# Kernel tuning notes

Hardware: AMD Instinct MI355X
Metric: run time of the kernel (lower is better)

The kernel has to match this reference:

```python
import jax, jax.numpy as jnp
import numpy as np

B, N, C = 2, 4096, 1024
HEADS = 16
BUCKET = 64
N_HASHES = 4
DH = C // HEADS
TOKEN_SELF_ATTN_VALUE = -5e4  # self-attention strongly discouraged (shared QK)


def setup_inputs() -> dict:
    key = jax.random.key(0)
    ks = jax.random.split(key, 8)
    s = 0.02
    n_buckets = N // BUCKET
    return {
        "queries": jax.random.normal(ks[0], (B, N, C), jnp.float32),
        "keys": jax.random.normal(ks[1], (B, N, C), jnp.float32),
        "values": jax.random.normal(ks[2], (B, N, C), jnp.float32),
        "attn_mask": jnp.zeros((1,), jnp.float32),
        "Wqk": jax.random.normal(ks[3], (C, C), jnp.float32) * s,
        "Wv": jax.random.normal(ks[4], (C, C), jnp.float32) * s,
        "Wout": jax.random.normal(ks[5], (C, C), jnp.float32) * s,
        "bout": jnp.zeros((C,), jnp.float32),
        # LSH random rotations, shared across batch and heads (reformer_pytorch default)
        "rotations": jax.random.normal(ks[6], (DH, N_HASHES, n_buckets // 2), jnp.float32),
        "tau": 1,
        "delta": 1,
    }


def _look_one_back(x):
    # concat each chunk with the previous chunk (wrap-around), along the kv axis
    extra = jnp.concatenate([x[:, -1:], x[:, :-1]], axis=1)
    return jnp.concatenate([x, extra], axis=2)


def _lsh_attention(qk, v, rotations, bucket_size, n_hashes):
    # qk, v: (bh, t, d); rotations: (d, n_hashes, n_buckets//2)
    bh, t, d = qk.shape
    n_buckets = t // bucket_size

    # --- hash vectors into buckets ---
    rotated = jnp.einsum('btf,fhi->bhti', qk, rotations)
    rotated = jnp.concatenate([rotated, -rotated], axis=-1)      # (bh, H, t, n_buckets)
    buckets = jnp.argmax(rotated, axis=-1)                       # (bh, H, t)
    offsets = (jnp.arange(n_hashes) * n_buckets)[None, :, None]
    buckets = (buckets + offsets).reshape(bh, n_hashes * t)

    # --- stable sort tokens by (bucket, position) ---
    ticker = jnp.arange(n_hashes * t)
    buckets_and_t = t * buckets + (ticker % t)[None, :]
    sticker = jnp.argsort(buckets_and_t, axis=-1)                # stable
    undo_sort = jnp.argsort(sticker, axis=-1)
    st = sticker % t                                             # original token idx per slot

    sqk = jnp.take_along_axis(qk, st[:, :, None], axis=1)
    sv = jnp.take_along_axis(v, st[:, :, None], axis=1)

    # --- chunk into n_hashes*n_buckets chunks of bucket_size ---
    n_chunks = n_hashes * n_buckets
    bq_t = st.reshape(bh, n_chunks, bucket_size)
    bqk = sqk.reshape(bh, n_chunks, bucket_size, d)
    bv = sv.reshape(bh, n_chunks, bucket_size, d)

    bq = bqk
    norm = jnp.linalg.norm(bqk, axis=-1, keepdims=True)
    bk = bqk / jnp.maximum(norm, 1e-12)                          # F.normalize, shared QK

    bk = _look_one_back(bk)
    bv = _look_one_back(bv)
    bkv_t = _look_one_back(bq_t)

    dots = jnp.einsum('bcie,bcje->bcij', bq, bk) * (d ** -0.5)   # (bh, nc, bs, 2*bs)
    self_mask = bq_t[..., :, None] == bkv_t[..., None, :]
    dots = jnp.where(self_mask, TOKEN_SELF_ATTN_VALUE, dots)

    dots_lse = jax.nn.logsumexp(dots, axis=-1, keepdims=True)
    probs = jnp.exp(dots - dots_lse)
    bo = jnp.einsum('bcij,bcje->bcie', probs, bv)

    # --- unsort and combine hash rounds by softmax over per-round logsumexps ---
    so = bo.reshape(bh, n_hashes * t, d)
    slogits = dots_lse.reshape(bh, n_hashes * t)
    o = jnp.take_along_axis(so, undo_sort[:, :, None], axis=1)
    logits = jnp.take_along_axis(slogits, undo_sort, axis=1)
    o = o.reshape(bh, n_hashes, t, d)
    logits = logits.reshape(bh, n_hashes, t, 1)
    w = jnp.exp(logits - jax.nn.logsumexp(logits, axis=1, keepdims=True))
    return jnp.sum(o * w, axis=1)                                # (bh, t, d)


def _forward(queries, Wqk, Wv, Wout, bout, rotations):
    b, n, c = queries.shape
    pad = (-n) % (BUCKET * 2)
    x = jnp.pad(queries, ((0, 0), (0, pad), (0, 0))) if pad else queries
    t = x.shape[1]
    qk = x @ Wqk.T
    v = x @ Wv.T
    qkh = qk.reshape(b, t, HEADS, DH).transpose(0, 2, 1, 3).reshape(b * HEADS, t, DH)
    vh = v.reshape(b, t, HEADS, DH).transpose(0, 2, 1, 3).reshape(b * HEADS, t, DH)
    oh = _lsh_attention(qkh, vh, rotations, BUCKET, N_HASHES)
    o = oh.reshape(b, HEADS, t, DH).transpose(0, 2, 1, 3).reshape(b, t, c)
    out = o @ Wout.T + bout
    return out[:, :n, :]


def reference(queries, keys, values, attn_mask, Wqk, Wv, Wout, bout, rotations, tau, delta):
    # keys/values/attn_mask/tau/delta are accepted but unused, as in the original layer
    return _forward(queries, Wqk, Wv, Wout, bout, rotations)
```

## Files before the change

kernel.cpp:

```cpp
#include <hip/hip_runtime.h>
#include <hip/hip_bf16.h>
#include <math.h>


__global__ __launch_bounds__(256) void sgemm128(const float* __restrict__ A,
                                                const float* __restrict__ W,
                                                float* __restrict__ out,
                                                int headLayout,
                                                const float* __restrict__ bias) {
    __shared__ float As[8][128];
    __shared__ float Bs[8][128];
    int tid = threadIdx.x;
    int tx = tid & 15, ty = tid >> 4;
    int m0 = blockIdx.x * 128, n0 = blockIdx.y * 128;
    int lr = tid >> 1;
    int lk = (tid & 1) * 4;
    float acc[8][8];
#pragma unroll
    for (int i = 0; i < 8; ++i)
#pragma unroll
        for (int j = 0; j < 8; ++j) acc[i][j] = 0.f;

    for (int k0 = 0; k0 < 1024; k0 += 8) {
        float4 av = *(const float4*)&A[(size_t)(m0 + lr) * 1024 + k0 + lk];
        float4 bv = *(const float4*)&W[(size_t)(n0 + lr) * 1024 + k0 + lk];
        __syncthreads();
        As[lk + 0][lr] = av.x; As[lk + 1][lr] = av.y;
        As[lk + 2][lr] = av.z; As[lk + 3][lr] = av.w;
        Bs[lk + 0][lr] = bv.x; Bs[lk + 1][lr] = bv.y;
        Bs[lk + 2][lr] = bv.z; Bs[lk + 3][lr] = bv.w;
        __syncthreads();
#pragma unroll
        for (int kk = 0; kk < 8; ++kk) {
            float a[8], b[8];
            *(float4*)&a[0] = *(const float4*)&As[kk][tx * 8];
            *(float4*)&a[4] = *(const float4*)&As[kk][tx * 8 + 4];
            *(float4*)&b[0] = *(const float4*)&Bs[kk][ty * 8];
            *(float4*)&b[4] = *(const float4*)&Bs[kk][ty * 8 + 4];
#pragma unroll
            for (int i = 0; i < 8; ++i)
#pragma unroll
                for (int j = 0; j < 8; ++j)
                    acc[i][j] = fmaf(a[i], b[j], acc[i][j]);
        }
    }
#pragma unroll
    for (int i = 0; i < 8; ++i) {
        int m = m0 + tx * 8 + i;
        int bb = m >> 12, t = m & 4095;
#pragma unroll
        for (int j = 0; j < 8; ++j) {
            int n = n0 + ty * 8 + j;
            float val = acc[i][j];
            if (bias) val += bias[n];
            if (headLayout) {
                out[(((size_t)(bb * 16 + (n >> 6))) * 4096 + t) * 64 + (n & 63)] = val;
            } else {
                out[(size_t)m * 1024 + n] = val;
            }
        }
    }
}

__global__ __launch_bounds__(256) void bucket32(const float* __restrict__ qk,
                                                const float* __restrict__ rot,
                                                int* __restrict__ keys) {
    int gid = blockIdx.x * 256 + threadIdx.x;
    int token = gid & 4095;
    int r = (gid >> 12) & 3;
    int bh = gid >> 14;
    const float* q = &qk[((size_t)bh * 4096 + token) * 64];
    float racc[32];
#pragma unroll
    for (int i = 0; i < 32; ++i) racc[i] = 0.f;
    for (int f = 0; f < 64; ++f) {
        float qv = q[f];
        const float* rp = &rot[f * 128 + r * 32];
#pragma unroll
        for (int i = 0; i < 32; ++i) racc[i] = fmaf(qv, rp[i], racc[i]);
    }
    float best = -INFINITY;
    int bi = 0;
#pragma unroll
    for (int i = 0; i < 32; ++i) { if (racc[i] > best) { best = racc[i]; bi = i; } }
#pragma unroll
    for (int i = 0; i < 32; ++i) { float x = -racc[i]; if (x > best) { best = x; bi = 32 + i; } }
    int bin = r * 64 + bi;
    keys[(size_t)bh * 16384 + r * 4096 + token] = bin * 4096 + token;
}

#define PST 257

__global__ __launch_bounds__(256) void countsort_kernel(const int* __restrict__ keys,
                                                        int* __restrict__ st_sorted) {
    __shared__ unsigned short pre[64 * PST];
    __shared__ unsigned char sbin[4096];
    __shared__ unsigned short sperm[4096];
    __shared__ int qsum[64 * 4];
    __shared__ int qoff[64 * 4];
    __shared__ int binOffset[64];

    int tid = threadIdx.x;
    int bh = blockIdx.x >> 2;
    int r = blockIdx.x & 3;
    const int* kb = &keys[(((size_t)bh * 4 + r) << 12)];

    for (int u = tid; u < 64 * PST; u += 256) pre[u] = 0;
    __syncthreads();

    int base = tid << 4;
#pragma unroll
    for (int u = 0; u < 4; ++u) {
        int4 kv = *(const int4*)&kb[base + u * 4];
        int b0 = (kv.x >> 12) & 63;
        int b1 = (kv.y >> 12) & 63;
        int b2 = (kv.z >> 12) & 63;
        int b3 = (kv.w >> 12) & 63;
        sbin[base + u * 4 + 0] = (unsigned char)b0;
        sbin[base + u * 4 + 1] = (unsigned char)b1;
        sbin[base + u * 4 + 2] = (unsigned char)b2;
        sbin[base + u * 4 + 3] = (unsigned char)b3;
        pre[b0 * PST + tid]++;
        pre[b1 * PST + tid]++;
        pre[b2 * PST + tid]++;
        pre[b3 * PST + tid]++;
    }
    __syncthreads();

    int b = tid & 63, q = tid >> 6;
    {
        int run = 0;
        for (int i = 0; i < 64; ++i) run += pre[b * PST + q * 64 + i];
        qsum[b * 4 + q] = run;
    }
    __syncthreads();

    if (tid < 64) {
        int s0 = qsum[tid * 4 + 0], s1 = qsum[tid * 4 + 1];
        int s2 = qsum[tid * 4 + 2], s3 = qsum[tid * 4 + 3];
        qoff[tid * 4 + 0] = 0;
        qoff[tid * 4 + 1] = s0;
        qoff[tid * 4 + 2] = s0 + s1;
        qoff[tid * 4 + 3] = s0 + s1 + s2;
        binOffset[tid] = s0 + s1 + s2 + s3;
    }
    __syncthreads();
    if (tid == 0) {
        int running = 0;
        for (int i = 0; i < 64; ++i) {
            int t = binOffset[i];
            binOffset[i] = running;
            running += t;
        }
    }
    __syncthreads();

    {
        int run2 = qoff[b * 4 + q];
        for (int i = 0; i < 64; ++i) {
            int idx = b * PST + q * 64 + i;
            int t = pre[idx];
            pre[idx] = (unsigned short)run2;
            run2 += t;
        }
    }
    __syncthreads();

#pragma unroll
    for (int k = 0; k < 16; ++k) {
        int bin = sbin[base + k];
        int off = pre[bin * PST + tid]++;
        sperm[binOffset[bin] + off] = (unsigned short)(base + k);
    }
    __syncthreads();

    int* ob = &st_sorted[(((size_t)bh * 4 + r) << 12)];
#pragma unroll
    for (int u = 0; u < 16; ++u) ob[u * 256 + tid] = (int)sperm[u * 256 + tid];
}

__global__ __launch_bounds__(256) void attn_kernel(const float* __restrict__ qk,
                                                   const float* __restrict__ v,
                                                   const int* __restrict__ st_sorted,
                                                   float* __restrict__ o4,
                                                   float* __restrict__ lse4) {
    __shared__ float bufA[128 * 68];
    __shared__ float vsl[128 * 68];
    __shared__ float red[64 * 17];
    __shared__ int posl[128];
    __shared__ float invl[128];

    int tid = threadIdx.x;
    int bh = blockIdx.x >> 8;
    int c = blockIdx.x & 255;
    int r = c >> 6;
    int pc = (c + 255) & 255;
    const int* stb = &st_sorted[(size_t)bh * 16384];
    if (tid < 64) posl[tid] = stb[c * 64 + tid];
    else if (tid < 128) posl[tid] = stb[pc * 64 + (tid - 64)];
    __syncthreads();

    float* kqt = bufA;
    for (int u = 0; u < 8; ++u) {
        int flat = u * 256 + tid;
        int row = flat >> 4;
        int f4 = (flat & 15) * 4;
        size_t gbase = ((size_t)bh * 4096 + posl[row]) * 64 + f4;
        float4 qv = *(const float4*)&qk[gbase];
        kqt[(f4 + 0) * 132 + row] = qv.x;
        kqt[(f4 + 1) * 132 + row] = qv.y;
        kqt[(f4 + 2) * 132 + row] = qv.z;
        kqt[(f4 + 3) * 132 + row] = qv.w;
        *(float4*)&vsl[row * 68 + f4] = *(const float4*)&v[gbase];
    }
    __syncthreads();

    if (tid < 128) {
        float ss = 0.f;
        for (int f = 0; f < 64; ++f) { float x = kqt[f * 132 + tid]; ss += x * x; }
        invl[tid] = 1.0f / fmaxf(sqrtf(ss), 1e-12f);
    }
    __syncthreads();

    int tx = tid & 15, ty = tid >> 4;
    float acc[4][8];
#pragma unroll
    for (int i = 0; i < 4; ++i)
#pragma unroll
        for (int j = 0; j < 8; ++j) acc[i][j] = 0.f;
    for (int f = 0; f < 64; ++f) {
        float a[4], b[8];
        *(float4*)a = *(const float4*)&kqt[f * 132 + tx * 4];
        *(float4*)&b[0] = *(const float4*)&kqt[f * 132 + ty * 8];
        *(float4*)&b[4] = *(const float4*)&kqt[f * 132 + ty * 8 + 4];
#pragma unroll
        for (int i = 0; i < 4; ++i)
#pragma unroll
            for (int j = 0; j < 8; ++j) acc[i][j] = fmaf(a[i], b[j], acc[i][j]);
    }

    int qp[4];
#pragma unroll
    for (int ii = 0; ii < 4; ++ii) qp[ii] = posl[tx * 4 + ii];
#pragma unroll
    for (int jj = 0; jj < 8; ++jj) {
        int j = ty * 8 + jj;
        float sc = invl[j] * 0.125f;
        int kp = posl[j];
#pragma unroll
        for (int ii = 0; ii < 4; ++ii) {
            float x = acc[ii][jj] * sc;
            acc[ii][jj] = (qp[ii] == kp) ? -5e4f : x;
        }
    }

#pragma unroll
    for (int ii = 0; ii < 4; ++ii) {
        float pm = acc[ii][0];
#pragma unroll
        for (int jj = 1; jj < 8; ++jj) pm = fmaxf(pm, acc[ii][jj]);
        red[(tx * 4 + ii) * 17 + ty] = pm;
    }
    __syncthreads();
    float m[4];
#pragma unroll
    for (int ii = 0; ii < 4; ++ii) {
        float mm = red[(tx * 4 + ii) * 17 + 0];
        for (int t = 1; t < 16; ++t) mm = fmaxf(mm, red[(tx * 4 + ii) * 17 + t]);
        m[ii] = mm;
    }
    __syncthreads();

    float* pT = bufA;
    float ps[4] = {0.f, 0.f, 0.f, 0.f};
#pragma unroll
    for (int jj = 0; jj < 8; ++jj) {
        int j = ty * 8 + jj;
#pragma unroll
        for (int ii = 0; ii < 4; ++ii) {
            float e = __expf(acc[ii][jj] - m[ii]);
            pT[j * 68 + tx * 4 + ii] = e;
            ps[ii] += e;
        }
    }
#pragma unroll
    for (int ii = 0; ii < 4; ++ii) red[(tx * 4 + ii) * 17 + ty] = ps[ii];
    __syncthreads();
    float l[4];
#pragma unroll
    for (int ii = 0; ii < 4; ++ii) {
        float s = 0.f;
        for (int t = 0; t < 16; ++t) s += red[(tx * 4 + ii) * 17 + t];
        l[ii] = s;
    }

    if (ty == 0) {
#pragma unroll
        for (int ii = 0; ii < 4; ++ii) {
            int i = tx * 4 + ii;
            lse4[((size_t)bh * 4 + r) * 4096 + posl[i]] = m[ii] + __logf(l[ii]);
        }
    }

    float acc2[4][4];
#pragma unroll
    for (int i = 0; i < 4; ++i)
#pragma unroll
        for (int j = 0; j < 4; ++j) acc2[i][j] = 0.f;
    for (int j = 0; j < 128; ++j) {
        float a[4], b[4];
        *(float4*)a = *(const float4*)&pT[j * 68 + tx * 4];
        *(float4*)b = *(const float4*)&vsl[j * 68 + ty * 4];
#pragma unroll
        for (int ii = 0; ii < 4; ++ii)
#pragma unroll
            for (int cc = 0; cc < 4; ++cc) acc2[ii][cc] = fmaf(a[ii], b[cc], acc2[ii][cc]);
    }
#pragma unroll
    for (int ii = 0; ii < 4; ++ii) {
        int i = tx * 4 + ii;
        float rl = 1.0f / l[ii];
        size_t ob = (((size_t)bh * 4 + r) * 4096 + posl[i]) * 64 + ty * 4;
        float4 ov;
        ov.x = acc2[ii][0] * rl;
        ov.y = acc2[ii][1] * rl;
        ov.z = acc2[ii][2] * rl;
        ov.w = acc2[ii][3] * rl;
        *(float4*)&o4[ob] = ov;
    }
}

__global__ __launch_bounds__(256) void combine_kernel(const float* __restrict__ o4,
                                                      const float* __restrict__ lse4,
                                                      float* __restrict__ o_bt) {
    int tid = threadIdx.x;
    int gt = blockIdx.x * 4 + (tid >> 6);
    int d = tid & 63;
    int bh = gt >> 12, p = gt & 4095;
    size_t base = ((size_t)bh * 4) * 4096 + p;
    float l0 = lse4[base];
    float l1 = lse4[base + 4096];
    float l2 = lse4[base + 8192];
    float l3 = lse4[base + 12288];
    float mm = fmaxf(fmaxf(l0, l1), fmaxf(l2, l3));
    float w0 = __expf(l0 - mm), w1 = __expf(l1 - mm);
    float w2 = __expf(l2 - mm), w3 = __expf(l3 - mm);
    float W = w0 + w1 + w2 + w3;
    size_t ob = (((size_t)bh * 4) * 4096 + p) * 64 + d;
    const size_t rs = (size_t)4096 * 64;
    float o = w0 * o4[ob]
            + w1 * o4[ob + rs]
            + w2 * o4[ob + 2 * rs]
            + w3 * o4[ob + 3 * rs];
    int b = bh >> 4, h = bh & 15;
    o_bt[((size_t)b * 4096 + p) * 1024 + h * 64 + d] = o / W;
}

extern "C" void kernel_launch(void* const* d_in, const int* in_sizes, int n_in,
                              void* d_out, int out_size, void* d_ws, size_t ws_size,
                              hipStream_t stream) {
    const float* x    = (const float*)d_in[0];
    const float* Wqk  = (const float*)d_in[4];
    const float* Wv   = (const float*)d_in[5];
    const float* Wout = (const float*)d_in[6];
    const float* bout = (const float*)d_in[7];
    const float* rot  = (const float*)d_in[8];
    float* out = (float*)d_out;

    char* ws = (char*)d_ws;
    float* qk32          = (float*)(ws);
    float* v             = (float*)(ws + 33554432);
    float* o4            = (float*)(ws + 67108864);
    float* lse4          = (float*)(ws + 201326592);
    int* keys            = (int*)(ws + 203423744);
    int* st_sorted       = (int*)(ws + 205520896);
    float* o_bt          = qk32;

    sgemm128<<<dim3(64, 8), 256, 0, stream>>>(x, Wqk, qk32, 1, nullptr);
    sgemm128<<<dim3(64, 8), 256, 0, stream>>>(x, Wv, v, 1, nullptr);
    bucket32<<<2048, 256, 0, stream>>>(qk32, rot, keys);
    countsort_kernel<<<128, 256, 0, stream>>>(keys, st_sorted);
    attn_kernel<<<8192, 256, 0, stream>>>(qk32, v, st_sorted, o4, lse4);
    combine_kernel<<<32768, 256, 0, stream>>>(o4, lse4, o_bt);
    sgemm128<<<dim3(64, 8), 256, 0, stream>>>(o_bt, Wout, out, 0, bout);
}
```

Baseline: 1.253 ms.

## Double-buffer SGEMM, swizzle LDS in attention, stream V from global

The SGEMM gets double-buffered shared tiles with a register prefetch and a single barrier per k-step, plus a block-index swizzle for L2 reuse. In the attention kernel, the transposed QK tile is XOR-swizzled to cut LDS bank conflicts, P stores become float4 writes, and the V staging in shared memory is dropped in favour of prefetched float4 reads from global inside the PV loop. The bucket kernel uses float4 loads of qk and a different block-to-token mapping. Together these target GEMM latency, LDS conflicts and shared-memory footprint, at the cost of scattered global V reads that are repeated by each thread row.

```diff
diff --git a/kernel.cpp b/kernel.cpp
--- a/kernel.cpp
+++ b/kernel.cpp
@@ -2,48 +2,69 @@
 #include <hip/hip_bf16.h>
 #include <math.h>
 
+
+#define SG_COMPUTE(BUF)                                                      \
+    {                                                                        \
+        _Pragma("unroll")                                                    \
+        for (int kk = 0; kk < 8; ++kk) {                                     \
+            float a[8], b[8];                                                \
+            *(float4*)&a[0] = *(const float4*)&As[BUF][kk][tx * 8];          \
+            *(float4*)&a[4] = *(const float4*)&As[BUF][kk][tx * 8 + 4];      \
+            *(float4*)&b[0] = *(const float4*)&Bs[BUF][kk][ty * 8];          \
+            *(float4*)&b[4] = *(const float4*)&Bs[BUF][kk][ty * 8 + 4];      \
+            _Pragma("unroll")                                                \
+            for (int i = 0; i < 8; ++i)                                      \
+                _Pragma("unroll")                                            \
+                for (int j = 0; j < 8; ++j)                                  \
+                    acc[i][j] = fmaf(a[i], b[j], acc[i][j]);                 \
+        }                                                                    \
+    }
 
 __global__ __launch_bounds__(256) void sgemm128(const float* __restrict__ A,
                                                 const float* __restrict__ W,
                                                 float* __restrict__ out,
                                                 int headLayout,
                                                 const float* __restrict__ bias) {
-    __shared__ float As[8][128];
-    __shared__ float Bs[8][128];
+    __shared__ float As[2][8][128];
+    __shared__ float Bs[2][8][128];
     int tid = threadIdx.x;
     int tx = tid & 15, ty = tid >> 4;
-    int m0 = blockIdx.x * 128, n0 = blockIdx.y * 128;
+    int id = blockIdx.x;
+    int swz = (id & 7) * 64 + (id >> 3);
+    int m0 = (swz & 63) * 128;
+    int n0 = (swz >> 6) * 128;
     int lr = tid >> 1;
     int lk = (tid & 1) * 4;
+    const float* pA = &A[(size_t)(m0 + lr) * 1024 + lk];
+    const float* pB = &W[(size_t)(n0 + lr) * 1024 + lk];
     float acc[8][8];
 #pragma unroll
     for (int i = 0; i < 8; ++i)
 #pragma unroll
         for (int j = 0; j < 8; ++j) acc[i][j] = 0.f;
 
-    for (int k0 = 0; k0 < 1024; k0 += 8) {
-        float4 av = *(const float4*)&A[(size_t)(m0 + lr) * 1024 + k0 + lk];
-        float4 bv = *(const float4*)&W[(size_t)(n0 + lr) * 1024 + k0 + lk];
+    float4 av = *(const float4*)&pA[0];
+    float4 bv = *(const float4*)&pB[0];
+    As[0][lk + 0][lr] = av.x; As[0][lk + 1][lr] = av.y;
+    As[0][lk + 2][lr] = av.z; As[0][lk + 3][lr] = av.w;
+    Bs[0][lk + 0][lr] = bv.x; Bs[0][lk + 1][lr] = bv.y;
+    Bs[0][lk + 2][lr] = bv.z; Bs[0][lk + 3][lr] = bv.w;
+    __syncthreads();
+
+    for (int it = 0; it < 127; ++it) {
+        int cur = it & 1;
+        int nxt = cur ^ 1;
+        av = *(const float4*)&pA[(it + 1) * 8];
+        bv = *(const float4*)&pB[(it + 1) * 8];
+        SG_COMPUTE(cur)
+        As[nxt][lk + 0][lr] = av.x; As[nxt][lk + 1][lr] = av.y;
+        As[nxt][lk + 2][lr] = av.z; As[nxt][lk + 3][lr] = av.w;
+        Bs[nxt][lk + 0][lr] = bv.x; Bs[nxt][lk + 1][lr] = bv.y;
+        Bs[nxt][lk + 2][lr] = bv.z; Bs[nxt][lk + 3][lr] = bv.w;
         __syncthreads();
-        As[lk + 0][lr] = av.x; As[lk + 1][lr] = av.y;
-        As[lk + 2][lr] = av.z; As[lk + 3][lr] = av.w;
-        Bs[lk + 0][lr] = bv.x; Bs[lk + 1][lr] = bv.y;
-        Bs[lk + 2][lr] = bv.z; Bs[lk + 3][lr] = bv.w;
-        __syncthreads();
-#pragma unroll
-        for (int kk = 0; kk < 8; ++kk) {
-            float a[8], b[8];
-            *(float4*)&a[0] = *(const float4*)&As[kk][tx * 8];
-            *(float4*)&a[4] = *(const float4*)&As[kk][tx * 8 + 4];
-            *(float4*)&b[0] = *(const float4*)&Bs[kk][ty * 8];
-            *(float4*)&b[4] = *(const float4*)&Bs[kk][ty * 8 + 4];
-#pragma unroll
-            for (int i = 0; i < 8; ++i)
-#pragma unroll
-                for (int j = 0; j < 8; ++j)
-                    acc[i][j] = fmaf(a[i], b[j], acc[i][j]);
-        }
-    }
+    }
+    SG_COMPUTE(1)
+
 #pragma unroll
     for (int i = 0; i < 8; ++i) {
         int m = m0 + tx * 8 + i;
@@ -61,23 +82,34 @@
         }
     }
 }
+#undef SG_COMPUTE
 
 __global__ __launch_bounds__(256) void bucket32(const float* __restrict__ qk,
                                                 const float* __restrict__ rot,
                                                 int* __restrict__ keys) {
-    int gid = blockIdx.x * 256 + threadIdx.x;
-    int token = gid & 4095;
-    int r = (gid >> 12) & 3;
-    int bh = gid >> 14;
+    int tid = threadIdx.x;
+    int blk = blockIdx.x;
+    int token = (blk & 15) * 256 + tid;
+    int r = (blk >> 4) & 3;
+    int bh = blk >> 6;
     const float* q = &qk[((size_t)bh * 4096 + token) * 64];
     float racc[32];
 #pragma unroll
     for (int i = 0; i < 32; ++i) racc[i] = 0.f;
-    for (int f = 0; f < 64; ++f) {
-        float qv = q[f];
-        const float* rp = &rot[f * 128 + r * 32];
-#pragma unroll
-        for (int i = 0; i < 32; ++i) racc[i] = fmaf(qv, rp[i], racc[i]);
+    for (int f0 = 0; f0 < 64; f0 += 4) {
+        float4 qv = *(const float4*)&q[f0];
+        const float* rp0 = &rot[(f0 + 0) * 128 + r * 32];
+        const float* rp1 = rp0 + 128;
+        const float* rp2 = rp0 + 256;
+        const float* rp3 = rp0 + 384;
+#pragma unroll
+        for (int i = 0; i < 32; ++i) racc[i] = fmaf(qv.x, rp0[i], racc[i]);
+#pragma unroll
+        for (int i = 0; i < 32; ++i) racc[i] = fmaf(qv.y, rp1[i], racc[i]);
+#pragma unroll
+        for (int i = 0; i < 32; ++i) racc[i] = fmaf(qv.z, rp2[i], racc[i]);
+#pragma unroll
+        for (int i = 0; i < 32; ++i) racc[i] = fmaf(qv.w, rp3[i], racc[i]);
     }
     float best = -INFINITY;
     int bi = 0;
@@ -185,7 +217,6 @@
                                                    float* __restrict__ o4,
                                                    float* __restrict__ lse4) {
     __shared__ float bufA[128 * 68];
-    __shared__ float vsl[128 * 68];
     __shared__ float red[64 * 17];
     __shared__ int posl[128];
     __shared__ float invl[128];
@@ -207,17 +238,21 @@
         int f4 = (flat & 15) * 4;
         size_t gbase = ((size_t)bh * 4096 + posl[row]) * 64 + f4;
         float4 qv = *(const float4*)&qk[gbase];
-        kqt[(f4 + 0) * 132 + row] = qv.x;
-        kqt[(f4 + 1) * 132 + row] = qv.y;
-        kqt[(f4 + 2) * 132 + row] = qv.z;
-        kqt[(f4 + 3) * 132 + row] = qv.w;
-        *(float4*)&vsl[row * 68 + f4] = *(const float4*)&v[gbase];
+        int rw = row ^ ((((f4 >> 2)) & 7) << 2);
+        kqt[(f4 + 0) * 132 + rw] = qv.x;
+        kqt[(f4 + 1) * 132 + rw] = qv.y;
+        kqt[(f4 + 2) * 132 + rw] = qv.z;
+        kqt[(f4 + 3) * 132 + rw] = qv.w;
     }
     __syncthreads();
 
     if (tid < 128) {
         float ss = 0.f;
-        for (int f = 0; f < 64; ++f) { float x = kqt[f * 132 + tid]; ss += x * x; }
+        for (int f = 0; f < 64; ++f) {
+            int s = ((f >> 2) & 7) << 2;
+            float x = kqt[f * 132 + (tid ^ s)];
+            ss += x * x;
+        }
         invl[tid] = 1.0f / fmaxf(sqrtf(ss), 1e-12f);
     }
     __syncthreads();
@@ -229,10 +264,11 @@
 #pragma unroll
         for (int j = 0; j < 8; ++j) acc[i][j] = 0.f;
     for (int f = 0; f < 64; ++f) {
+        int s = ((f >> 2) & 7) << 2;
         float a[4], b[8];
-        *(float4*)a = *(const float4*)&kqt[f * 132 + tx * 4];
-        *(float4*)&b[0] = *(const float4*)&kqt[f * 132 + ty * 8];
-        *(float4*)&b[4] = *(const float4*)&kqt[f * 132 + ty * 8 + 4];
+        *(float4*)a = *(const float4*)&kqt[f * 132 + ((tx * 4) ^ s)];
+        *(float4*)&b[0] = *(const float4*)&kqt[f * 132 + ((ty * 8) ^ s)];
+        *(float4*)&b[4] = *(const float4*)&kqt[f * 132 + ((ty * 8 + 4) ^ s)];
 #pragma unroll
         for (int i = 0; i < 4; ++i)
 #pragma unroll
@@ -276,12 +312,13 @@
 #pragma unroll
     for (int jj = 0; jj < 8; ++jj) {
         int j = ty * 8 + jj;
-#pragma unroll
-        for (int ii = 0; ii < 4; ++ii) {
-            float e = __expf(acc[ii][jj] - m[ii]);
-            pT[j * 68 + tx * 4 + ii] = e;
-            ps[ii] += e;
-        }
+        float e0 = __expf(acc[0][jj] - m[0]);
+        float e1 = __expf(acc[1][jj] - m[1]);
+        float e2 = __expf(acc[2][jj] - m[2]);
+        float e3 = __expf(acc[3][jj] - m[3]);
+        ps[0] += e0; ps[1] += e1; ps[2] += e2; ps[3] += e3;
+        float4 ev; ev.x = e0; ev.y = e1; ev.z = e2; ev.w = e3;
+        *(float4*)&pT[j * 68 + tx * 4] = ev;
     }
 #pragma unroll
     for (int ii = 0; ii < 4; ++ii) red[(tx * 4 + ii) * 17 + ty] = ps[ii];
@@ -302,19 +339,51 @@
         }
     }
 
+    const float* vb = v + (size_t)bh * 4096 * 64 + ty * 4;
     float acc2[4][4];
 #pragma unroll
     for (int i = 0; i < 4; ++i)
 #pragma unroll
         for (int j = 0; j < 4; ++j) acc2[i][j] = 0.f;
-    for (int j = 0; j < 128; ++j) {
-        float a[4], b[4];
-        *(float4*)a = *(const float4*)&pT[j * 68 + tx * 4];
-        *(float4*)b = *(const float4*)&vsl[j * 68 + ty * 4];
-#pragma unroll
-        for (int ii = 0; ii < 4; ++ii)
-#pragma unroll
-            for (int cc = 0; cc < 4; ++cc) acc2[ii][cc] = fmaf(a[ii], b[cc], acc2[ii][cc]);
+
+    float4 p0 = *(const float4*)&vb[(size_t)posl[0] * 64];
+    float4 p1 = *(const float4*)&vb[(size_t)posl[1] * 64];
+    float4 p2 = *(const float4*)&vb[(size_t)posl[2] * 64];
+    float4 p3 = *(const float4*)&vb[(size_t)posl[3] * 64];
+    for (int j0 = 0; j0 < 128; j0 += 4) {
+        float4 c0 = p0, c1 = p1, c2 = p2, c3 = p3;
+        if (j0 + 4 < 128) {
+            p0 = *(const float4*)&vb[(size_t)posl[j0 + 4] * 64];
+            p1 = *(const float4*)&vb[(size_t)posl[j0 + 5] * 64];
+            p2 = *(const float4*)&vb[(size_t)posl[j0 + 6] * 64];
+            p3 = *(const float4*)&vb[(size_t)posl[j0 + 7] * 64];
+        }
+#define PVSTEP(JJ, CV)                                                       \
+        {                                                                    \
+            float a_[4];                                                     \
+            *(float4*)a_ = *(const float4*)&pT[(j0 + (JJ)) * 68 + tx * 4];   \
+            acc2[0][0] = fmaf(a_[0], CV.x, acc2[0][0]);                      \
+            acc2[0][1] = fmaf(a_[0], CV.y, acc2[0][1]);                      \
+            acc2[0][2] = fmaf(a_[0], CV.z, acc2[0][2]);                      \
+            acc2[0][3] = fmaf(a_[0], CV.w, acc2[0][3]);                      \
+            acc2[1][0] = fmaf(a_[1], CV.x, acc2[1][0]);                      \
+            acc2[1][1] = fmaf(a_[1], CV.y, acc2[1][1]);                      \
+            acc2[1][2] = fmaf(a_[1], CV.z, acc2[1][2]);                      \
+            acc2[1][3] = fmaf(a_[1], CV.w, acc2[1][3]);                      \
+            acc2[2][0] = fmaf(a_[2], CV.x, acc2[2][0]);                      \
+            acc2[2][1] = fmaf(a_[2], CV.y, acc2[2][1]);                      \
+            acc2[2][2] = fmaf(a_[2], CV.z, acc2[2][2]);                      \
+            acc2[2][3] = fmaf(a_[2], CV.w, acc2[2][3]);                      \
+            acc2[3][0] = fmaf(a_[3], CV.x, acc2[3][0]);                      \
+            acc2[3][1] = fmaf(a_[3], CV.y, acc2[3][1]);                      \
+            acc2[3][2] = fmaf(a_[3], CV.z, acc2[3][2]);                      \
+            acc2[3][3] = fmaf(a_[3], CV.w, acc2[3][3]);                      \
+        }
+        PVSTEP(0, c0)
+        PVSTEP(1, c1)
+        PVSTEP(2, c2)
+        PVSTEP(3, c3)
+#undef PVSTEP
     }
 #pragma unroll
     for (int ii = 0; ii < 4; ++ii) {
@@ -376,11 +445,11 @@
     int* st_sorted       = (int*)(ws + 205520896);
     float* o_bt          = qk32;
 
-    sgemm128<<<dim3(64, 8), 256, 0, stream>>>(x, Wqk, qk32, 1, nullptr);
-    sgemm128<<<dim3(64, 8), 256, 0, stream>>>(x, Wv, v, 1, nullptr);
+    sgemm128<<<512, 256, 0, stream>>>(x, Wqk, qk32, 1, nullptr);
+    sgemm128<<<512, 256, 0, stream>>>(x, Wv, v, 1, nullptr);
     bucket32<<<2048, 256, 0, stream>>>(qk32, rot, keys);
     countsort_kernel<<<128, 256, 0, stream>>>(keys, st_sorted);
     attn_kernel<<<8192, 256, 0, stream>>>(qk32, v, st_sorted, o4, lse4);
     combine_kernel<<<32768, 256, 0, stream>>>(o4, lse4, o_bt);
-    sgemm128<<<dim3(64, 8), 256, 0, stream>>>(o_bt, Wout, out, 0, bout);
-}
+    sgemm128<<<512, 256, 0, stream>>>(o_bt, Wout, out, 0, bout);
+}
```

Result: faster. 1.165 ms (-7.0%).
